# Kernel optimization log

Measured on AMD Instinct MI355X. Metric: run time of the kernel, lower is better.

Reference implementation:

```python
import jax, jax.numpy as jnp
import numpy as np

D_MODEL = 1024
NUM_HEADS = 16
HEAD_DIM = D_MODEL // NUM_HEADS
FF_HIDDEN = 2 * D_MODEL
EPS = 1e-5


def _layernorm(x, g, b):
    mu = jnp.mean(x, axis=-1, keepdims=True)
    var = jnp.var(x, axis=-1, keepdims=True)
    return (x - mu) * jax.lax.rsqrt(var + EPS) * g + b


def setup_inputs() -> dict:
    key = jax.random.key(0)
    ks = jax.random.split(key, 12)
    s = lambda fan_in: 1.0 / np.sqrt(fan_in)
    return {
        "x": jax.random.normal(ks[0], (4, 2048, D_MODEL), dtype=jnp.float32),
        "qkv_w": jax.random.uniform(ks[1], (D_MODEL, 3 * D_MODEL), minval=-s(D_MODEL), maxval=s(D_MODEL)),
        "qkv_b": jax.random.uniform(ks[2], (3 * D_MODEL,), minval=-s(D_MODEL), maxval=s(D_MODEL)),
        "out_w": jax.random.uniform(ks[3], (D_MODEL, D_MODEL), minval=-s(D_MODEL), maxval=s(D_MODEL)),
        "out_b": jax.random.uniform(ks[4], (D_MODEL,), minval=-s(D_MODEL), maxval=s(D_MODEL)),
        "ff1_w": jax.random.uniform(ks[5], (D_MODEL, FF_HIDDEN), minval=-s(D_MODEL), maxval=s(D_MODEL)),
        "ff1_b": jax.random.uniform(ks[6], (FF_HIDDEN,), minval=-s(D_MODEL), maxval=s(D_MODEL)),
        "ff2_w": jax.random.uniform(ks[7], (FF_HIDDEN, D_MODEL), minval=-s(FF_HIDDEN), maxval=s(FF_HIDDEN)),
        "ff2_b": jax.random.uniform(ks[8], (D_MODEL,), minval=-s(FF_HIDDEN), maxval=s(FF_HIDDEN)),
        "ln1_g": jnp.ones((D_MODEL,), jnp.float32),
        "ln1_b": jnp.zeros((D_MODEL,), jnp.float32),
        "ln2_g": jnp.ones((D_MODEL,), jnp.float32),
        "ln2_b": jnp.zeros((D_MODEL,), jnp.float32),
    }


def reference(x, qkv_w, qkv_b, out_w, out_b, ff1_w, ff1_b, ff2_w, ff2_b, ln1_g, ln1_b, ln2_g, ln2_b):
    B, L, _ = x.shape
    scale = HEAD_DIM ** -0.5
    # pre-norm attention
    h = _layernorm(x, ln1_g, ln1_b)
    qkv = h @ qkv_w + qkv_b  # [B,L,3D]
    q, k, v = jnp.split(qkv, 3, axis=-1)
    reshape = lambda t: t.reshape(B, L, NUM_HEADS, HEAD_DIM).transpose(0, 2, 1, 3)  # [B,H,L,Dh]
    q, k, v = reshape(q), reshape(k), reshape(v)
    attn = jnp.einsum('bhqd,bhkd->bhqk', q, k) * scale  # [B,H,L,L]
    attn = jax.nn.softmax(attn, axis=-1)
    ctx = jnp.einsum('bhqk,bhkd->bhqd', attn, v)
    ctx = ctx.transpose(0, 2, 1, 3).reshape(B, L, D_MODEL)
    attended = ctx @ out_w + out_b
    x = x + attended
    # pre-norm FFN with exact GELU (torch default)
    h2 = _layernorm(x, ln2_g, ln2_b)
    ff = jax.nn.gelu(h2 @ ff1_w + ff1_b, approximate=False) @ ff2_w + ff2_b
    return x + ff
```

## Files before the change

### kernel.cpp

```cpp
#include <hip/hip_runtime.h>

#define AS1 __attribute__((address_space(1)))
#define AS3 __attribute__((address_space(3)))

typedef unsigned short u16;
typedef __bf16 bf16x8 __attribute__((ext_vector_type(8)));
typedef float floatx4 __attribute__((ext_vector_type(4)));
typedef float floatx16 __attribute__((ext_vector_type(16)));
typedef u16 u16x8 __attribute__((ext_vector_type(8)));
typedef u16 u16x4 __attribute__((ext_vector_type(4)));
typedef unsigned uintx4 __attribute__((ext_vector_type(4)));

__device__ __forceinline__ float bf2f(u16 u) { return __uint_as_float(((unsigned)u) << 16); }
__device__ __forceinline__ u16 f2bf(float f) {
    unsigned u = __float_as_uint(f);
    u += 0x7FFFu + ((u >> 16) & 1u);
    return (u16)(u >> 16);
}
__device__ __forceinline__ unsigned packbf2(float f0, float f1) {
    return __builtin_amdgcn_perm(__float_as_uint(f1), __float_as_uint(f0), 0x07060302u);
}
__device__ __forceinline__ void gl_lds16(const u16* g, u16* l) {
    __builtin_amdgcn_global_load_lds((const AS1 void*)g, (AS3 void*)l, 16, 0, 0);
}

__global__ __launch_bounds__(256) void transpose_f2b(const float* __restrict__ in,
                                                     u16* __restrict__ out, int R, int C) {
    __shared__ u16 t[32][33];
    const int c0 = blockIdx.x * 32, r0 = blockIdx.y * 32;
    const int tx = threadIdx.x, ty = threadIdx.y;
#pragma unroll
    for (int i = 0; i < 4; i++)
        t[ty + i * 8][tx] = f2bf(in[(size_t)(r0 + ty + i * 8) * C + c0 + tx]);
    __syncthreads();
#pragma unroll
    for (int i = 0; i < 4; i++) out[(size_t)(c0 + ty + i * 8) * R + r0 + tx] = t[tx][ty + i * 8];
}

__global__ __launch_bounds__(256) void ln_k(const float* __restrict__ x, const float* __restrict__ g,
                                            const float* __restrict__ b, u16* __restrict__ out) {
    const int row = blockIdx.x, tid = threadIdx.x;
    const float4 xv = *(const float4*)(x + (size_t)row * 1024 + tid * 4);
    float f[4] = {xv.x, xv.y, xv.z, xv.w};
    float s1 = 0.f, s2 = 0.f;
#pragma unroll
    for (int e = 0; e < 4; e++) {
        s1 += f[e];
        s2 += f[e] * f[e];
    }
#pragma unroll
    for (int off = 32; off >= 1; off >>= 1) {
        s1 += __shfl_down(s1, off);
        s2 += __shfl_down(s2, off);
    }
    __shared__ float w1[4], w2[4];
    const int wave = tid >> 6, lane = tid & 63;
    if (lane == 0) { w1[wave] = s1; w2[wave] = s2; }
    __syncthreads();
    s1 = w1[0] + w1[1] + w1[2] + w1[3];
    s2 = w2[0] + w2[1] + w2[2] + w2[3];
    const float mu = s1 * (1.0f / 1024.0f);
    const float var = s2 * (1.0f / 1024.0f) - mu * mu;
    const float rs = rsqrtf(var + 1e-5f);
    const float4 gv = *(const float4*)(g + tid * 4);
    const float4 bv = *(const float4*)(b + tid * 4);
    const float gf[4] = {gv.x, gv.y, gv.z, gv.w}, bff[4] = {bv.x, bv.y, bv.z, bv.w};
    u16x4 o;
#pragma unroll
    for (int e = 0; e < 4; e++) o[e] = f2bf((f[e] - mu) * rs * gf[e] + bff[e]);
    *(u16x4*)(out + (size_t)row * 1024 + tid * 4) = o;
}

template <int GELU, int RESID, int F32OUT>
__global__ __launch_bounds__(256) void gemm_bt(const u16* __restrict__ A, const u16* __restrict__ Bt,
                                               const float* __restrict__ bias,
                                               const float* __restrict__ resid, void* __restrict__ Cv,
                                               int M, int N, int K, int lda) {
    __shared__ u16 Al[128 * 32];
    __shared__ u16 Bl[128 * 32];
    const int tid = threadIdx.x;
    const int wave = tid >> 6, lane = tid & 63;
    const int g16 = lane >> 4, l16 = lane & 15;
    const int m0 = blockIdx.y * 128, n0 = blockIdx.x * 128;
    const int wm = (wave >> 1) * 64, wn = (wave & 1) * 64;

    floatx4 acc[4][4] = {};

    const u16* Ag = A + (size_t)(m0 + (lane >> 2)) * lda + (lane & 3) * 8;
    const u16* Bg = Bt + (size_t)(n0 + (lane >> 2)) * K + (lane & 3) * 8;

    for (int k0 = 0; k0 < K; k0 += 32) {
        __syncthreads();
#pragma unroll
        for (int i = 0; i < 2; i++) {
            const int ro = 16 * (wave * 2 + i);
            gl_lds16(Ag + (size_t)ro * lda + k0, &Al[(wave * 2 + i) * 512]);
            gl_lds16(Bg + (size_t)ro * K + k0, &Bl[(wave * 2 + i) * 512]);
        }
        __syncthreads();
        bf16x8 af[4], bfr[4];
#pragma unroll
        for (int i = 0; i < 4; i++) af[i] = *(const bf16x8*)&Al[(wm + i * 16 + l16) * 32 + g16 * 8];
#pragma unroll
        for (int j = 0; j < 4; j++) bfr[j] = *(const bf16x8*)&Bl[(wn + j * 16 + l16) * 32 + g16 * 8];
#pragma unroll
        for (int i = 0; i < 4; i++)
#pragma unroll
            for (int j = 0; j < 4; j++)
                acc[i][j] = __builtin_amdgcn_mfma_f32_16x16x32_bf16(af[i], bfr[j], acc[i][j], 0, 0, 0);
    }

    float bv[4];
#pragma unroll
    for (int j = 0; j < 4; j++) bv[j] = bias[n0 + wn + j * 16 + l16];
#pragma unroll
    for (int i = 0; i < 4; i++) {
#pragma unroll
        for (int r = 0; r < 4; r++) {
            const int gm = m0 + wm + i * 16 + g16 * 4 + r;
            const size_t ro = (size_t)gm * N;
#pragma unroll
            for (int j = 0; j < 4; j++) {
                const int gn = n0 + wn + j * 16 + l16;
                float v = acc[i][j][r] + bv[j];
                if (GELU) v = 0.5f * v * (1.0f + erff(v * 0.70710678118654752f));
                if (RESID) v += resid[ro + gn];
                if (F32OUT)
                    ((float*)Cv)[ro + gn] = v;
                else
                    ((u16*)Cv)[ro + gn] = f2bf(v);
            }
        }
    }
}

__global__ __launch_bounds__(256) void attn_prep(u16* __restrict__ qkv, u16* __restrict__ Vsw) {
    __shared__ u16 Tl[64][72];
    const int bh = blockIdx.y, b = bh >> 4, h = bh & 15;
    const int kt = blockIdx.x * 64;
    const int t = threadIdx.x;
    const size_t qbase = (size_t)b * 2048 * 3072;
    const int r = t >> 2, cpi = (t & 3) * 2;

    u16* krow = qkv + qbase + (size_t)(kt + r) * 3072 + 1024 + h * 64;
    *(u16x8*)&Tl[r][cpi * 8] = *(const u16x8*)(krow + cpi * 8);
    *(u16x8*)&Tl[r][(cpi + 1) * 8] = *(const u16x8*)(krow + (cpi + 1) * 8);
    __syncthreads();
    {
        const u16x8 a = *(const u16x8*)&Tl[r][(cpi ^ (r & 7)) * 8];
        const u16x8 c = *(const u16x8*)&Tl[r][((cpi + 1) ^ (r & 7)) * 8];
        *(u16x8*)(krow + cpi * 8) = a;
        *(u16x8*)(krow + (cpi + 1) * 8) = c;
    }
    __syncthreads();
    const u16* vrow = qkv + qbase + (size_t)(kt + r) * 3072 + 2048 + h * 64;
    *(u16x8*)&Tl[r][cpi * 8] = *(const u16x8*)(vrow + cpi * 8);
    *(u16x8*)&Tl[r][(cpi + 1) * 8] = *(const u16x8*)(vrow + (cpi + 1) * 8);
    __syncthreads();
    {
        const int d = r;
        u16* dst = Vsw + ((size_t)bh * 64 + d) * 2048 + kt;
#pragma unroll
        for (int i = 0; i < 2; i++) {
            const int cp = cpi + i;
            const int c = cp ^ (d & 7);
            u16x8 tmp;
#pragma unroll
            for (int e = 0; e < 8; e++) tmp[e] = Tl[c * 8 + e][d];
            *(u16x8*)(dst + cp * 8) = tmp;
        }
    }
}

__global__ __launch_bounds__(256, 4) void attn_k(u16* __restrict__ qkv, const u16* __restrict__ Vsw) {
    __shared__ u16 Kl[2][64 * 64];
    __shared__ u16 Vt[2][64 * 64];
    const int tid = threadIdx.x;
    const int w = tid >> 6, lane = tid & 63;
    const int l31 = lane & 31, half = lane >> 5, swz = lane & 7;
    const int bh = blockIdx.y, b = bh >> 4, h = bh & 15;
    const int q0 = blockIdx.x * 128 + w * 32;
    const size_t qbase = (size_t)b * 2048 * 3072;
    const size_t vbase = (size_t)bh * 64 * 2048;

    bf16x8 bq[4];
    {
        const u16* qp = qkv + qbase + (size_t)(q0 + l31) * 3072 + h * 64;
        const float sc = 0.125f * 1.44269504088896340736f;
#pragma unroll
        for (int kd = 0; kd < 4; kd++) {
            const u16x8 raw = *(const u16x8*)(qp + kd * 16 + half * 8);
            u16 tmp[8];
#pragma unroll
            for (int e = 0; e < 8; e++) tmp[e] = f2bf(bf2f(raw[e]) * sc);
            bq[kd] = *(const bf16x8*)tmp;
        }
    }

    floatx16 accO[2] = {};
    float lsum = 0.f;

    auto stage = [&](int buf, int kt) {
#pragma unroll
        for (int i = 0; i < 2; i++) {
            const int rr = w * 16 + i * 8 + (lane >> 3);
            gl_lds16(qkv + qbase + (size_t)(kt + rr) * 3072 + 1024 + h * 64 + (lane & 7) * 8,
                     &Kl[buf][(w * 16 + i * 8) * 64]);
            gl_lds16(Vsw + vbase + (size_t)rr * 2048 + kt + (lane & 7) * 8,
                     &Vt[buf][(w * 16 + i * 8) * 64]);
        }
    };

    stage(0, 0);
    __syncthreads();
    int buf = 0;
    for (int kt = 0; kt < 2048; kt += 64) {
        if (kt + 64 < 2048) stage(buf ^ 1, kt + 64);

        floatx16 accS[2] = {};
#pragma unroll
        for (int kb = 0; kb < 2; kb++)
#pragma unroll
            for (int kd = 0; kd < 4; kd++) {
                const bf16x8 ak =
                    *(const bf16x8*)&Kl[buf][(kb * 32 + l31) * 64 + ((kd * 2 + half) ^ swz) * 8];
                accS[kb] = __builtin_amdgcn_mfma_f32_32x32x16_bf16(ak, bq[kd], accS[kb], 0, 0, 0);
            }

        uintx4 Pf[4];
#pragma unroll
        for (int kb = 0; kb < 2; kb++) {
            float E[16];
#pragma unroll
            for (int e = 0; e < 16; e++) {
                E[e] = exp2f(accS[kb][e]);
                lsum += E[e];
            }
#pragma unroll
            for (int kp = 0; kp < 2; kp++) {
                unsigned x0 = packbf2(E[8 * kp + 0], E[8 * kp + 1]);
                unsigned x1 = packbf2(E[8 * kp + 2], E[8 * kp + 3]);
                unsigned y0 = packbf2(E[8 * kp + 4], E[8 * kp + 5]);
                unsigned y1 = packbf2(E[8 * kp + 6], E[8 * kp + 7]);
                asm volatile("v_permlane32_swap_b32 %0, %1" : "+v"(x0), "+v"(y0));
                asm volatile("v_permlane32_swap_b32 %0, %1" : "+v"(x1), "+v"(y1));
                uintx4 f;
                f[0] = x0; f[1] = x1; f[2] = y0; f[3] = y1;
                Pf[kb * 2 + kp] = f;
            }
        }

#pragma unroll
        for (int kd = 0; kd < 4; kd++) {
            const bf16x8 bp = __builtin_bit_cast(bf16x8, Pf[kd]);
#pragma unroll
            for (int db = 0; db < 2; db++) {
                const bf16x8 av =
                    *(const bf16x8*)&Vt[buf][(db * 32 + l31) * 64 + ((kd * 2 + half) ^ swz) * 8];
                accO[db] = __builtin_amdgcn_mfma_f32_32x32x16_bf16(av, bp, accO[db], 0, 0, 0);
            }
        }
        __syncthreads();
        buf ^= 1;
    }

    lsum += __shfl_xor(lsum, 32);
    const float rinv = 1.0f / lsum;
    u16* cw = qkv + qbase + (size_t)(q0 + l31) * 3072 + 2048 + h * 64;
#pragma unroll
    for (int db = 0; db < 2; db++)
#pragma unroll
        for (int rg = 0; rg < 4; rg++) {
            const int d0 = db * 32 + 8 * rg + 4 * half;
            u16x4 o;
#pragma unroll
            for (int rr2 = 0; rr2 < 4; rr2++) o[rr2] = f2bf(accO[db][rg * 4 + rr2] * rinv);
            *(u16x4*)(cw + d0) = o;
        }
}

extern "C" void kernel_launch(void* const* d_in, const int* in_sizes, int n_in, void* d_out,
                              int out_size, void* d_ws, size_t ws_size, hipStream_t stream) {
    const float* x = (const float*)d_in[0];
    const float* qkv_w = (const float*)d_in[1];
    const float* qkv_b = (const float*)d_in[2];
    const float* out_w = (const float*)d_in[3];
    const float* out_b = (const float*)d_in[4];
    const float* ff1_w = (const float*)d_in[5];
    const float* ff1_b = (const float*)d_in[6];
    const float* ff2_w = (const float*)d_in[7];
    const float* ff2_b = (const float*)d_in[8];
    const float* ln1_g = (const float*)d_in[9];
    const float* ln1_b = (const float*)d_in[10];
    const float* ln2_g = (const float*)d_in[11];
    const float* ln2_b = (const float*)d_in[12];
    float* out = (float*)d_out;

    char* ws = (char*)d_ws;
    u16* qkvT = (u16*)(ws);
    u16* outT = (u16*)(ws + 6291456);
    u16* ff1T = (u16*)(ws + 8388608);
    u16* ff2T = (u16*)(ws + 12582912);
    u16* hbuf = (u16*)(ws + 16777216);
    u16* big  = (u16*)(ws + 33554432);

    transpose_f2b<<<dim3(96, 32), dim3(32, 8), 0, stream>>>(qkv_w, qkvT, 1024, 3072);
    transpose_f2b<<<dim3(32, 32), dim3(32, 8), 0, stream>>>(out_w, outT, 1024, 1024);
    transpose_f2b<<<dim3(64, 32), dim3(32, 8), 0, stream>>>(ff1_w, ff1T, 1024, 2048);
    transpose_f2b<<<dim3(32, 64), dim3(32, 8), 0, stream>>>(ff2_w, ff2T, 2048, 1024);

    ln_k<<<8192, 256, 0, stream>>>(x, ln1_g, ln1_b, hbuf);
    gemm_bt<0, 0, 0><<<dim3(24, 64), 256, 0, stream>>>(hbuf, qkvT, qkv_b, nullptr, big, 8192, 3072, 1024, 1024);
    attn_prep<<<dim3(32, 64), 256, 0, stream>>>(big, hbuf);
    attn_k<<<dim3(16, 64), 256, 0, stream>>>(big, hbuf);
    gemm_bt<0, 1, 1><<<dim3(8, 64), 256, 0, stream>>>(big + 2048, outT, out_b, x, out, 8192, 1024, 1024, 3072);
    ln_k<<<8192, 256, 0, stream>>>(out, ln2_g, ln2_b, hbuf);
    gemm_bt<1, 0, 0><<<dim3(16, 64), 256, 0, stream>>>(hbuf, ff1T, ff1_b, nullptr, big, 8192, 2048, 1024, 1024);
    gemm_bt<0, 1, 1><<<dim3(8, 64), 256, 0, stream>>>(big, ff2T, ff2_b, out, out, 8192, 1024, 2048, 2048);
}
```

Before: 488.3 us.

## Double-buffer GEMM LDS, swizzle LDS columns, fold K swizzle into QKV epilogue, merge transposes

The GEMM now double-buffers its LDS tiles so the global-to-LDS load of the next K step overlaps the MFMAs on the current one, with one barrier per iteration. It also XOR-swizzles the LDS chunk layout to cut bank conflicts and sets a launch-bounds occupancy hint. The K-tile swizzle that attn_prep used to apply in a separate read-modify-write pass is now written directly by the QKV GEMM epilogue. The four weight transposes are merged into a single launch. Together these target load latency, LDS conflicts, extra memory traffic and launch overhead. The cost is twice the LDS per block, which may limit occupancy.

```diff
diff --git a/kernel.cpp b/kernel.cpp
--- a/kernel.cpp
+++ b/kernel.cpp
@@ -24,10 +24,25 @@
     __builtin_amdgcn_global_load_lds((const AS1 void*)g, (AS3 void*)l, 16, 0, 0);
 }
 
-__global__ __launch_bounds__(256) void transpose_f2b(const float* __restrict__ in,
-                                                     u16* __restrict__ out, int R, int C) {
+__global__ __launch_bounds__(256) void transpose_all(const float* __restrict__ w0, u16* __restrict__ o0,
+                                                     const float* __restrict__ w1, u16* __restrict__ o1,
+                                                     const float* __restrict__ w2, u16* __restrict__ o2,
+                                                     const float* __restrict__ w3, u16* __restrict__ o3) {
     __shared__ u16 t[32][33];
-    const int c0 = blockIdx.x * 32, r0 = blockIdx.y * 32;
+    int blk = blockIdx.x;
+    const float* in;
+    u16* out;
+    int R, C, bx, by;
+    if (blk < 3072) {
+        in = w0; out = o0; R = 1024; C = 3072; bx = blk % 96; by = blk / 96;
+    } else if (blk < 4096) {
+        blk -= 3072; in = w1; out = o1; R = 1024; C = 1024; bx = blk % 32; by = blk / 32;
+    } else if (blk < 6144) {
+        blk -= 4096; in = w2; out = o2; R = 1024; C = 2048; bx = blk % 64; by = blk / 64;
+    } else {
+        blk -= 6144; in = w3; out = o3; R = 2048; C = 1024; bx = blk % 32; by = blk / 32;
+    }
+    const int c0 = bx * 32, r0 = by * 32;
     const int tx = threadIdx.x, ty = threadIdx.y;
 #pragma unroll
     for (int i = 0; i < 4; i++)
@@ -71,43 +86,54 @@
     *(u16x4*)(out + (size_t)row * 1024 + tid * 4) = o;
 }
 
-template <int GELU, int RESID, int F32OUT>
-__global__ __launch_bounds__(256) void gemm_bt(const u16* __restrict__ A, const u16* __restrict__ Bt,
-                                               const float* __restrict__ bias,
-                                               const float* __restrict__ resid, void* __restrict__ Cv,
-                                               int M, int N, int K, int lda) {
-    __shared__ u16 Al[128 * 32];
-    __shared__ u16 Bl[128 * 32];
+template <int GELU, int RESID, int F32OUT, int KSWZ>
+__global__ __launch_bounds__(256, 4) void gemm_bt(const u16* __restrict__ A, const u16* __restrict__ Bt,
+                                                  const float* __restrict__ bias,
+                                                  const float* __restrict__ resid, void* __restrict__ Cv,
+                                                  int M, int N, int K, int lda) {
+    __shared__ u16 Al[2][128 * 32];
+    __shared__ u16 Bl[2][128 * 32];
     const int tid = threadIdx.x;
     const int wave = tid >> 6, lane = tid & 63;
     const int g16 = lane >> 4, l16 = lane & 15;
     const int m0 = blockIdx.y * 128, n0 = blockIdx.x * 128;
     const int wm = (wave >> 1) * 64, wn = (wave & 1) * 64;
+    const int csw = (l16 >> 1) & 3;
 
     floatx4 acc[4][4] = {};
 
-    const u16* Ag = A + (size_t)(m0 + (lane >> 2)) * lda + (lane & 3) * 8;
-    const u16* Bg = Bt + (size_t)(n0 + (lane >> 2)) * K + (lane & 3) * 8;
-
-    for (int k0 = 0; k0 < K; k0 += 32) {
-        __syncthreads();
+    const int scs = ((lane & 3) ^ ((lane >> 3) & 3)) * 8;
+    const u16* Ag = A + (size_t)(m0 + (lane >> 2)) * lda + scs;
+    const u16* Bg = Bt + (size_t)(n0 + (lane >> 2)) * K + scs;
+
+    auto stage = [&](int buf, int k0) {
 #pragma unroll
         for (int i = 0; i < 2; i++) {
             const int ro = 16 * (wave * 2 + i);
-            gl_lds16(Ag + (size_t)ro * lda + k0, &Al[(wave * 2 + i) * 512]);
-            gl_lds16(Bg + (size_t)ro * K + k0, &Bl[(wave * 2 + i) * 512]);
-        }
-        __syncthreads();
+            gl_lds16(Ag + (size_t)ro * lda + k0, &Al[buf][(wave * 2 + i) * 512]);
+            gl_lds16(Bg + (size_t)ro * K + k0, &Bl[buf][(wave * 2 + i) * 512]);
+        }
+    };
+
+    stage(0, 0);
+    __syncthreads();
+    int buf = 0;
+    for (int k0 = 0; k0 < K; k0 += 32) {
+        if (k0 + 32 < K) stage(buf ^ 1, k0 + 32);
         bf16x8 af[4], bfr[4];
 #pragma unroll
-        for (int i = 0; i < 4; i++) af[i] = *(const bf16x8*)&Al[(wm + i * 16 + l16) * 32 + g16 * 8];
-#pragma unroll
-        for (int j = 0; j < 4; j++) bfr[j] = *(const bf16x8*)&Bl[(wn + j * 16 + l16) * 32 + g16 * 8];
+        for (int i = 0; i < 4; i++)
+            af[i] = *(const bf16x8*)&Al[buf][(wm + i * 16 + l16) * 32 + ((g16 ^ csw) << 3)];
+#pragma unroll
+        for (int j = 0; j < 4; j++)
+            bfr[j] = *(const bf16x8*)&Bl[buf][(wn + j * 16 + l16) * 32 + ((g16 ^ csw) << 3)];
 #pragma unroll
         for (int i = 0; i < 4; i++)
 #pragma unroll
             for (int j = 0; j < 4; j++)
                 acc[i][j] = __builtin_amdgcn_mfma_f32_16x16x32_bf16(af[i], bfr[j], acc[i][j], 0, 0, 0);
+        __syncthreads();
+        buf ^= 1;
     }
 
     float bv[4];
@@ -121,10 +147,11 @@
             const size_t ro = (size_t)gm * N;
 #pragma unroll
             for (int j = 0; j < 4; j++) {
-                const int gn = n0 + wn + j * 16 + l16;
+                int gn = n0 + wn + j * 16 + l16;
                 float v = acc[i][j][r] + bv[j];
                 if (GELU) v = 0.5f * v * (1.0f + erff(v * 0.70710678118654752f));
                 if (RESID) v += resid[ro + gn];
+                if (KSWZ && ((gn >> 10) == 1)) gn ^= (gm & 7) << 3;
                 if (F32OUT)
                     ((float*)Cv)[ro + gn] = v;
                 else
@@ -134,7 +161,7 @@
     }
 }
 
-__global__ __launch_bounds__(256) void attn_prep(u16* __restrict__ qkv, u16* __restrict__ Vsw) {
+__global__ __launch_bounds__(256) void attn_prep(const u16* __restrict__ qkv, u16* __restrict__ Vsw) {
     __shared__ u16 Tl[64][72];
     const int bh = blockIdx.y, b = bh >> 4, h = bh & 15;
     const int kt = blockIdx.x * 64;
@@ -142,17 +169,6 @@
     const size_t qbase = (size_t)b * 2048 * 3072;
     const int r = t >> 2, cpi = (t & 3) * 2;
 
-    u16* krow = qkv + qbase + (size_t)(kt + r) * 3072 + 1024 + h * 64;
-    *(u16x8*)&Tl[r][cpi * 8] = *(const u16x8*)(krow + cpi * 8);
-    *(u16x8*)&Tl[r][(cpi + 1) * 8] = *(const u16x8*)(krow + (cpi + 1) * 8);
-    __syncthreads();
-    {
-        const u16x8 a = *(const u16x8*)&Tl[r][(cpi ^ (r & 7)) * 8];
-        const u16x8 c = *(const u16x8*)&Tl[r][((cpi + 1) ^ (r & 7)) * 8];
-        *(u16x8*)(krow + cpi * 8) = a;
-        *(u16x8*)(krow + (cpi + 1) * 8) = c;
-    }
-    __syncthreads();
     const u16* vrow = qkv + qbase + (size_t)(kt + r) * 3072 + 2048 + h * 64;
     *(u16x8*)&Tl[r][cpi * 8] = *(const u16x8*)(vrow + cpi * 8);
     *(u16x8*)&Tl[r][(cpi + 1) * 8] = *(const u16x8*)(vrow + (cpi + 1) * 8);
@@ -304,17 +320,14 @@
     u16* hbuf = (u16*)(ws + 16777216);
     u16* big  = (u16*)(ws + 33554432);
 
-    transpose_f2b<<<dim3(96, 32), dim3(32, 8), 0, stream>>>(qkv_w, qkvT, 1024, 3072);
-    transpose_f2b<<<dim3(32, 32), dim3(32, 8), 0, stream>>>(out_w, outT, 1024, 1024);
-    transpose_f2b<<<dim3(64, 32), dim3(32, 8), 0, stream>>>(ff1_w, ff1T, 1024, 2048);
-    transpose_f2b<<<dim3(32, 64), dim3(32, 8), 0, stream>>>(ff2_w, ff2T, 2048, 1024);
+    transpose_all<<<8192, dim3(32, 8), 0, stream>>>(qkv_w, qkvT, out_w, outT, ff1_w, ff1T, ff2_w, ff2T);
 
     ln_k<<<8192, 256, 0, stream>>>(x, ln1_g, ln1_b, hbuf);
-    gemm_bt<0, 0, 0><<<dim3(24, 64), 256, 0, stream>>>(hbuf, qkvT, qkv_b, nullptr, big, 8192, 3072, 1024, 1024);
+    gemm_bt<0, 0, 0, 1><<<dim3(24, 64), 256, 0, stream>>>(hbuf, qkvT, qkv_b, nullptr, big, 8192, 3072, 1024, 1024);
     attn_prep<<<dim3(32, 64), 256, 0, stream>>>(big, hbuf);
     attn_k<<<dim3(16, 64), 256, 0, stream>>>(big, hbuf);
-    gemm_bt<0, 1, 1><<<dim3(8, 64), 256, 0, stream>>>(big + 2048, outT, out_b, x, out, 8192, 1024, 1024, 3072);
+    gemm_bt<0, 1, 1, 0><<<dim3(8, 64), 256, 0, stream>>>(big + 2048, outT, out_b, x, out, 8192, 1024, 1024, 3072);
     ln_k<<<8192, 256, 0, stream>>>(out, ln2_g, ln2_b, hbuf);
-    gemm_bt<1, 0, 0><<<dim3(16, 64), 256, 0, stream>>>(hbuf, ff1T, ff1_b, nullptr, big, 8192, 2048, 1024, 1024);
-    gemm_bt<0, 1, 1><<<dim3(8, 64), 256, 0, stream>>>(big, ff2T, ff2_b, out, out, 8192, 1024, 2048, 2048);
-}
+    gemm_bt<1, 0, 0, 0><<<dim3(16, 64), 256, 0, stream>>>(hbuf, ff1T, ff1_b, nullptr, big, 8192, 2048, 1024, 1024);
+    gemm_bt<0, 1, 1, 0><<<dim3(8, 64), 256, 0, stream>>>(big, ff2T, ff2_b, out, out, 8192, 1024, 2048, 2048);
+}
```

Result: faster. 461.2 us (-5.6%).
